# Kernel tuning notes

Hardware: AMD Instinct MI355X
Metric: run time of the kernel (lower is better)

Reference implementation:

```python
import jax, jax.numpy as jnp
import numpy as np

BN_EPS = 1e-5
POOL_TARGETS = (1500, 750, 375)


def mesh_conv(x, nb, W, g, b):
    # x: (E, C), nb: (E, 4), W: (5*C, Cout)
    E, C = x.shape
    n = x[jnp.clip(nb, 0, E - 1)]              # (E, 4, C) gather
    p1 = jnp.sort(n[:, :2, :], axis=1)          # symmetrize face-pair 1
    p2 = jnp.sort(n[:, 2:, :], axis=1)          # symmetrize face-pair 2
    feat = jnp.concatenate([x, p1[:, 0], p1[:, 1], p2[:, 0], p2[:, 1]], axis=1)  # (E, 5C)
    h = feat @ W                                # (E, Cout)
    mu = h.mean(axis=0)
    var = h.var(axis=0)                         # biased var (BatchNorm training stats)
    h = (h - mu) * jax.lax.rsqrt(var + BN_EPS) * g + b
    return jax.nn.relu(h)


def mesh_pool(x, nb, target):
    E = x.shape[0]
    scores = jnp.linalg.norm(x, axis=1)
    keep = jnp.sort(jnp.argsort(-scores)[:target])          # (target,) sorted kept edges
    x_pool = x[keep]
    remap = jnp.full((E,), -1, dtype=jnp.int32).at[keep].set(jnp.arange(target, dtype=jnp.int32))
    nbr = remap[jnp.clip(nb[keep], 0, E - 1)]               # (target, 4)
    self_idx = jnp.broadcast_to(jnp.arange(target, dtype=jnp.int32)[:, None], nbr.shape)
    nb_pool = jnp.where(nbr < 0, self_idx, nbr)
    return x_pool, nb_pool, keep


def mesh_unpool(x_coarse, keep, E_fine):
    # keep is sorted ascending; nearest kept edge by integer index distance
    # (ties -> lower index, matching torch argmin-first semantics).
    idx = jnp.arange(E_fine)
    pos = jnp.searchsorted(keep, idx)
    K = keep.shape[0]
    left = jnp.clip(pos - 1, 0, K - 1)
    right = jnp.clip(pos, 0, K - 1)
    dl = jnp.abs(idx - keep[left])
    dr = jnp.abs(idx - keep[right])
    nn_idx = jnp.where(dl <= dr, left, right)
    return x_coarse[nn_idx]                                 # kept edges map to themselves (d=0)


def setup_inputs() -> dict:
    key = jax.random.key(0)
    ks = jax.random.split(key, 20)
    E = 200000
    x = jax.random.normal(ks[0], (E, 5), dtype=jnp.float32)
    nb = jax.random.randint(ks[1], (E, 4), 0, E, dtype=jnp.int64)

    def lin(k, cin, cout):
        return (jax.random.normal(k, (cin, cout), dtype=jnp.float32) * 0.05)

    dims = [(5, 64), (64, 128), (128, 256), (256, 512), (768, 256), (384, 128), (192, 64)]
    names = ['e1', 'e2', 'e3', 'e4', 'd3', 'd2', 'd1']
    inp = {'x': x, 'nb': nb}
    for i, ((cin, cout), nm) in enumerate(zip(dims, names)):
        inp['W_' + nm] = lin(ks[2 + i], cin * 5, cout)
        inp['g_' + nm] = jnp.ones((cout,), dtype=jnp.float32)
        inp['b_' + nm] = jnp.zeros((cout,), dtype=jnp.float32)
    inp['W_head'] = lin(ks[12], 64, 4)
    inp['bias_head'] = jnp.zeros((4,), dtype=jnp.float32)
    return inp


def _forward(x, nb,
             W_e1, g_e1, b_e1, W_e2, g_e2, b_e2, W_e3, g_e3, b_e3, W_e4, g_e4, b_e4,
             W_d3, g_d3, b_d3, W_d2, g_d2, b_d2, W_d1, g_d1, b_d1,
             W_head, bias_head):
    e1 = mesh_conv(x, nb, W_e1, g_e1, b_e1)
    e1p, nb1, keep1 = mesh_pool(e1, nb, POOL_TARGETS[0])
    e2 = mesh_conv(e1p, nb1, W_e2, g_e2, b_e2)
    e2p, nb2, keep2 = mesh_pool(e2, nb1, POOL_TARGETS[1])
    e3 = mesh_conv(e2p, nb2, W_e3, g_e3, b_e3)
    e3p, nb3, keep3 = mesh_pool(e3, nb2, POOL_TARGETS[2])
    e4 = mesh_conv(e3p, nb3, W_e4, g_e4, b_e4)
    d3 = mesh_unpool(e4, keep3, e3.shape[0])
    d3 = mesh_conv(jnp.concatenate([d3, e3], axis=1), nb2, W_d3, g_d3, b_d3)
    d2 = mesh_unpool(d3, keep2, e2.shape[0])
    d2 = mesh_conv(jnp.concatenate([d2, e2], axis=1), nb1, W_d2, g_d2, b_d2)
    d1 = mesh_unpool(d2, keep1, e1.shape[0])
    d1 = mesh_conv(jnp.concatenate([d1, e1], axis=1), nb, W_d1, g_d1, b_d1)
    return d1 @ W_head + bias_head


def reference(x, nb,
              W_e1, g_e1, b_e1, W_e2, g_e2, b_e2, W_e3, g_e3, b_e3, W_e4, g_e4, b_e4,
              W_d3, g_d3, b_d3, W_d2, g_d2, b_d2, W_d1, g_d1, b_d1,
              W_head, bias_head):
    return _forward(x, nb,
                    W_e1, g_e1, b_e1, W_e2, g_e2, b_e2, W_e3, g_e3, b_e3, W_e4, g_e4, b_e4,
                    W_d3, g_d3, b_d3, W_d2, g_d2, b_d2, W_d1, g_d1, b_d1,
                    W_head, bias_head)
```

## Files before the change

kernel.cpp:

```cpp
#include <hip/hip_runtime.h>
#include <stdint.h>

typedef unsigned long long u64;
typedef unsigned int u32;
typedef unsigned short ushort_t;

#define FI __device__ __forceinline__

static constexpr float BN_EPS_F = 1e-5f;
static constexpr int E0 = 200000;
static constexpr int T1 = 1500, T2 = 750, T3 = 375;
static constexpr int CAND_CAP = 4096;
static constexpr int NB_KEEP = (E0 + 1023) / 1024;

typedef __attribute__((ext_vector_type(8))) short short8;
typedef __attribute__((ext_vector_type(4))) float f32x4;

FI int iclampi(int v, int lo, int hi) { return v < lo ? lo : (v > hi ? hi : v); }

FI ushort_t f2b(float f) {
  u32 u = __float_as_uint(f);
  u32 r = (u + 0x7FFFu + ((u >> 16) & 1u)) >> 16;
  return (ushort_t)r;
}

FI void u16minmax(const uint4& va, const uint4& vb, uint4& lo, uint4& hi) {
  const ushort_t* a = (const ushort_t*)&va;
  const ushort_t* b = (const ushort_t*)&vb;
  ushort_t* l = (ushort_t*)&lo;
  ushort_t* h = (ushort_t*)&hi;
  #pragma unroll
  for (int i = 0; i < 8; i++) {
    ushort_t x = a[i], y = b[i];
    l[i] = x < y ? x : y;
    h[i] = x < y ? y : x;
  }
}

FI int nearest_keep(const int* __restrict__ keep, int K, int idx) {
  int lo = 0, hi = K;
  while (lo < hi) { int mid = (lo + hi) >> 1; if (keep[mid] < idx) lo = mid + 1; else hi = mid; }
  int l = lo - 1; l = l < 0 ? 0 : (l > K - 1 ? K - 1 : l);
  int r = lo;     r = r < 0 ? 0 : (r > K - 1 ? K - 1 : r);
  int dl = idx - keep[l]; dl = dl < 0 ? -dl : dl;
  int dr = idx - keep[r]; dr = dr < 0 ? -dr : dr;
  return (dl <= dr) ? l : r;
}

FI int bsearch_eq(const int* __restrict__ keep, int K, int v) {
  int lo = 0, hi = K;
  while (lo < hi) { int mid = (lo + hi) >> 1; if (keep[mid] < v) lo = mid + 1; else hi = mid; }
  if (lo < K && keep[lo] == v) return lo;
  return -1;
}

template<int C, int Cout, int BR, int BC, int KT, int TR, int TC, int KSPLIT,
         bool FUSE_STATS>
__global__ __launch_bounds__((BR / TR) * (BC / TC))
void conv_kernel(const float* __restrict__ X,
                 const int* __restrict__ nb, int E,
                 const float* __restrict__ W,
                 float* __restrict__ H, float* __restrict__ stats)
{
  constexpr int NTH = (BR / TR) * (BC / TC);
  constexpr int VK = 5 * KT;
  constexpr int KC = C / KSPLIT;
  static_assert(KC % KT == 0, "KC % KT");

  const int row0 = blockIdx.x * BR;
  const int col0 = blockIdx.y * BC;
  const int c_begin = (KSPLIT > 1) ? (int)blockIdx.z * KC : 0;

  __shared__ float As[VK][BR];
  __shared__ float Bs[VK][BC];
  __shared__ int rowsS[5][BR];
  __shared__ float red[FUSE_STATS ? 2 * (BR / TR) * BC : 1];

  const int tid = threadIdx.x;

  for (int q = tid; q < BR; q += NTH) {
    int r = row0 + q;
    int rr[5];
    if (r < E) {
      rr[0] = r;
      #pragma unroll
      for (int j = 0; j < 4; j++) {
        int v = nb[(size_t)r * 4 + j];
        rr[1 + j] = iclampi(v, 0, E - 1);
      }
    } else {
      #pragma unroll
      for (int j = 0; j < 5; j++) rr[j] = -1;
    }
    #pragma unroll
    for (int j = 0; j < 5; j++) rowsS[j][q] = rr[j];
  }

  float acc[TR][TC];
  #pragma unroll
  for (int i = 0; i < TR; i++)
    #pragma unroll
    for (int j = 0; j < TC; j++) acc[i][j] = 0.f;

  const int tr = tid / (BC / TC);
  const int tc = tid % (BC / TC);
  const int rA = tr * TR;
  const int cB = tc * TC;

  for (int c0 = c_begin; c0 < c_begin + KC; c0 += KT) {
    __syncthreads();
    for (int q = tid; q < VK * (BC / 4); q += NTH) {
      int kk = q / (BC / 4);
      int c4 = q % (BC / 4);
      int p = kk / KT, t = kk % KT;
      float4 wv = *(const float4*)&W[(size_t)(p * C + c0 + t) * Cout + col0 + c4 * 4];
      *(float4*)&Bs[kk][c4 * 4] = wv;
    }
    for (int q = tid; q < BR * KT; q += NTH) {
      int t = q % KT, rq = q / KT;
      int c = c0 + t;
      float s0 = 0.f, a1 = 0.f, a2 = 0.f, a3 = 0.f, a4 = 0.f;
      if (rowsS[0][rq] >= 0) {
        float v0, v1, v2, v3;
        s0 = X[(size_t)rowsS[0][rq] * C + c];
        v0 = X[(size_t)rowsS[1][rq] * C + c];
        v1 = X[(size_t)rowsS[2][rq] * C + c];
        v2 = X[(size_t)rowsS[3][rq] * C + c];
        v3 = X[(size_t)rowsS[4][rq] * C + c];
        a1 = fminf(v0, v1); a2 = fmaxf(v0, v1);
        a3 = fminf(v2, v3); a4 = fmaxf(v2, v3);
      }
      As[0 * KT + t][rq] = s0;
      As[1 * KT + t][rq] = a1;
      As[2 * KT + t][rq] = a2;
      As[3 * KT + t][rq] = a3;
      As[4 * KT + t][rq] = a4;
    }
    __syncthreads();

    for (int kk = 0; kk < VK; kk++) {
      float a[TR], b[TC];
      #pragma unroll
      for (int i = 0; i < TR; i++) a[i] = As[kk][rA + i];
      #pragma unroll
      for (int j = 0; j < TC; j++) b[j] = Bs[kk][cB + j];
      #pragma unroll
      for (int i = 0; i < TR; i++)
        #pragma unroll
        for (int j = 0; j < TC; j++)
          acc[i][j] = fmaf(a[i], b[j], acc[i][j]);
    }
  }

  #pragma unroll
  for (int i = 0; i < TR; i++) {
    int r = row0 + rA + i;
    if (r < E) {
      if constexpr (KSPLIT > 1) {
        #pragma unroll
        for (int j = 0; j < TC; j++)
          atomicAdd(&H[(size_t)r * Cout + col0 + cB + j], acc[i][j]);
      } else {
        #pragma unroll
        for (int j = 0; j < TC; j += 4) {
          float4 v = make_float4(acc[i][j], acc[i][j + 1], acc[i][j + 2], acc[i][j + 3]);
          *(float4*)&H[(size_t)r * Cout + col0 + cB + j] = v;
        }
      }
    }
  }

  if constexpr (FUSE_STATS) {
    float s[TC], q2[TC];
    #pragma unroll
    for (int j = 0; j < TC; j++) { s[j] = 0.f; q2[j] = 0.f; }
    #pragma unroll
    for (int i = 0; i < TR; i++) {
      int r = row0 + rA + i;
      if (r < E) {
        #pragma unroll
        for (int j = 0; j < TC; j++) { float v = acc[i][j]; s[j] += v; q2[j] += v * v; }
      }
    }
    __syncthreads();
    float* redS = &red[0];
    float* redQ = &red[(BR / TR) * BC];
    #pragma unroll
    for (int j = 0; j < TC; j++) {
      redS[tr * BC + cB + j] = s[j];
      redQ[tr * BC + cB + j] = q2[j];
    }
    __syncthreads();
    for (int col = tid; col < BC; col += NTH) {
      float ts = 0.f, tq = 0.f;
      for (int g = 0; g < BR / TR; g++) { ts += redS[g * BC + col]; tq += redQ[g * BC + col]; }
      atomicAdd(&stats[col0 + col], ts);
      atomicAdd(&stats[Cout + col0 + col], tq);
    }
  }
}

__global__ __launch_bounds__(256)
void e1_conv_kernel(const float* __restrict__ X, const int* __restrict__ nb,
                    const float* __restrict__ W,
                    float* __restrict__ H, float* __restrict__ stats)
{
  __shared__ float As[25][128];
  __shared__ float Bs[25][64];
  __shared__ float red[2 * 32 * 64];

  const int tid = threadIdx.x;
  const int row0 = (int)blockIdx.x * 128;

  if (tid < 128) {
    int r = row0 + tid; if (r > E0 - 1) r = E0 - 1;
    int rs[5];
    rs[0] = r;
    #pragma unroll
    for (int j = 0; j < 4; j++) rs[1 + j] = iclampi((int)nb[(size_t)r * 4 + j], 0, E0 - 1);
    float v[5][5];
    #pragma unroll
    for (int j = 0; j < 5; j++) {
      const float* src = &X[(size_t)rs[j] * 5];
      float4 a = *(const float4*)src;
      v[j][0] = a.x; v[j][1] = a.y; v[j][2] = a.z; v[j][3] = a.w;
      v[j][4] = src[4];
    }
    #pragma unroll
    for (int c = 0; c < 5; c++) {
      As[0 * 5 + c][tid] = v[0][c];
      As[1 * 5 + c][tid] = fminf(v[1][c], v[2][c]);
      As[2 * 5 + c][tid] = fmaxf(v[1][c], v[2][c]);
      As[3 * 5 + c][tid] = fminf(v[3][c], v[4][c]);
      As[4 * 5 + c][tid] = fmaxf(v[3][c], v[4][c]);
    }
  } else {
    for (int q = tid - 128; q < 25 * 16; q += 128) {
      int k = q / 16, c4 = q % 16;
      float4 wv = *(const float4*)&W[(size_t)k * 64 + c4 * 4];
      *(float4*)&Bs[k][c4 * 4] = wv;
    }
  }
  __syncthreads();

  const int tr = tid >> 3;
  const int tc = tid & 7;
  const int rA = tr * 4;
  const int cB = tc * 8;

  float acc[4][8];
  #pragma unroll
  for (int i = 0; i < 4; i++)
    #pragma unroll
    for (int j = 0; j < 8; j++) acc[i][j] = 0.f;

  for (int k = 0; k < 25; k++) {
    float a[4], b[8];
    #pragma unroll
    for (int i = 0; i < 4; i++) a[i] = As[k][rA + i];
    #pragma unroll
    for (int j = 0; j < 8; j++) b[j] = Bs[k][cB + j];
    #pragma unroll
    for (int i = 0; i < 4; i++)
      #pragma unroll
      for (int j = 0; j < 8; j++)
        acc[i][j] = fmaf(a[i], b[j], acc[i][j]);
  }

  float s[8], q2[8];
  #pragma unroll
  for (int j = 0; j < 8; j++) { s[j] = 0.f; q2[j] = 0.f; }
  #pragma unroll
  for (int i = 0; i < 4; i++) {
    int r = row0 + rA + i;
    if (r < E0) {
      #pragma unroll
      for (int j = 0; j < 8; j += 4) {
        float4 v = make_float4(acc[i][j], acc[i][j + 1], acc[i][j + 2], acc[i][j + 3]);
        *(float4*)&H[(size_t)r * 64 + cB + j] = v;
      }
      #pragma unroll
      for (int j = 0; j < 8; j++) { float v = acc[i][j]; s[j] += v; q2[j] += v * v; }
    }
  }
  __syncthreads();
  float* redS = &red[0];
  float* redQ = &red[32 * 64];
  #pragma unroll
  for (int j = 0; j < 8; j++) {
    redS[tr * 64 + cB + j] = s[j];
    redQ[tr * 64 + cB + j] = q2[j];
  }
  __syncthreads();
  for (int col = tid; col < 64; col += 256) {
    float ts = 0.f, tq = 0.f;
    for (int g = 0; g < 32; g++) { ts += redS[g * 64 + col]; tq += redQ[g * 64 + col]; }
    atomicAdd(&stats[col], ts);
    atomicAdd(&stats[64 + col], tq);
  }
}

template<int C, int Cout, int KSPLIT>
__global__ __launch_bounds__(128)
void mfma_conv_kernel(const ushort_t* __restrict__ src,
                      const int* __restrict__ nb, int E,
                      const ushort_t* __restrict__ Wt,
                      float* __restrict__ H)
{
  constexpr int NCC_T = C / 32;
  constexpr int NCC = NCC_T / KSPLIT;
  static_assert(NCC_T % KSPLIT == 0, "NCC_T % KSPLIT");
  __shared__ int rows[5][32];

  const int tid = threadIdx.x;
  const int lane = tid & 63;
  const int wv = tid >> 6;
  const int l15 = lane & 15;
  const int quad = lane >> 4;
  const int row0 = (int)blockIdx.x * 32;
  const int col0 = (int)blockIdx.y * 64;
  const int cc0 = (KSPLIT > 1) ? (int)blockIdx.z * NCC : 0;

  if (tid < 32) {
    int r = row0 + tid; if (r > E - 1) r = E - 1;
    rows[0][tid] = r;
    #pragma unroll
    for (int j = 0; j < 4; j++) rows[1 + j][tid] = iclampi(nb[(size_t)r * 4 + j], 0, E - 1);
  }
  __syncthreads();

  const int rr = wv * 16 + l15;
  int r5[5];
  #pragma unroll
  for (int j = 0; j < 5; j++) r5[j] = rows[j][rr];

  f32x4 acc[4];
  #pragma unroll
  for (int ni = 0; ni < 4; ni++) acc[ni] = (f32x4){0.f, 0.f, 0.f, 0.f};

  uint4 raw[2][5];
  auto loadcc = [&](int par, int cc2) {
    int cb = (cc0 + cc2) * 32 + quad * 8;
    #pragma unroll
    for (int j = 0; j < 5; j++)
      raw[par][j] = *(const uint4*)&src[(size_t)r5[j] * C + cb];
  };

  loadcc(0, 0);
  #pragma unroll
  for (int cc = 0; cc < NCC; cc++) {
    const int par = cc & 1;
    if (cc + 1 < NCC) loadcc(par ^ 1, cc + 1);
    short8 a[5];
    a[0] = *(short8*)&raw[par][0];
    {
      uint4 lo, hi;
      u16minmax(raw[par][1], raw[par][2], lo, hi);
      a[1] = *(short8*)&lo; a[2] = *(short8*)&hi;
    }
    {
      uint4 lo, hi;
      u16minmax(raw[par][3], raw[par][4], lo, hi);
      a[3] = *(short8*)&lo; a[4] = *(short8*)&hi;
    }
    #pragma unroll
    for (int p = 0; p < 5; p++) {
      #pragma unroll
      for (int ni = 0; ni < 4; ni++) {
        short8 bf = *(const short8*)&Wt[((size_t)(p * Cout + col0 + ni * 16 + l15)) * C + (cc0 + cc) * 32 + quad * 8];
        acc[ni] = __builtin_amdgcn_mfma_f32_16x16x32_bf16(a[p], bf, acc[ni], 0, 0, 0);
      }
    }
  }

  #pragma unroll
  for (int reg = 0; reg < 4; reg++) {
    int r = row0 + wv * 16 + quad * 4 + reg;
    if (r < E) {
      #pragma unroll
      for (int ni = 0; ni < 4; ni++) {
        if constexpr (KSPLIT > 1)
          atomicAdd(&H[(size_t)r * Cout + col0 + ni * 16 + l15], acc[ni][reg]);
        else
          H[(size_t)r * Cout + col0 + ni * 16 + l15] = acc[ni][reg];
      }
    }
  }
}

__global__ __launch_bounds__(256, 4)
void d1_mfma_kernel(const ushort_t* __restrict__ d2b, const ushort_t* __restrict__ e1b,
                    const int* __restrict__ nn1, const int* __restrict__ nb,
                    const ushort_t* __restrict__ Wt,
                    float* __restrict__ H, float* __restrict__ stats)
{
  __shared__ int rowsD[5][128];
  __shared__ int rowsS[5][128];

  const int tid = threadIdx.x;
  const int lane = tid & 63;
  const int wv = tid >> 6;
  const int l15 = lane & 15;
  const int quad = lane >> 4;
  const int row0 = (int)blockIdx.x * 128;

  if (tid < 128) {
    int r = row0 + tid; if (r > E0 - 1) r = E0 - 1;
    int rs[5];
    rs[0] = r;
    #pragma unroll
    for (int j = 0; j < 4; j++) rs[1 + j] = iclampi((int)nb[(size_t)r * 4 + j], 0, E0 - 1);
    #pragma unroll
    for (int j = 0; j < 5; j++) { rowsS[j][tid] = rs[j]; rowsD[j][tid] = nn1[rs[j]]; }
  }
  __syncthreads();

  f32x4 acc[8];
  #pragma unroll
  for (int mi = 0; mi < 8; mi++) acc[mi] = (f32x4){0.f, 0.f, 0.f, 0.f};

  for (int cc = 0; cc < 6; cc++) {
    const bool fromD = cc < 4;
    const ushort_t* __restrict__ src = fromD ? d2b : e1b;
    const int stride = fromD ? 128 : 64;
    const int cbase = (fromD ? cc * 32 : (cc - 4) * 32) + quad * 8;

    short8 bf[5];
    #pragma unroll
    for (int p = 0; p < 5; p++)
      bf[p] = *(const short8*)&Wt[((size_t)(p * 64 + wv * 16 + l15)) * 192 + cc * 32 + quad * 8];

    #pragma unroll 2
    for (int mi = 0; mi < 8; mi++) {
      int rr = mi * 16 + l15;
      int r0, r1, r2, r3, r4;
      if (fromD) {
        r0 = rowsD[0][rr]; r1 = rowsD[1][rr]; r2 = rowsD[2][rr];
        r3 = rowsD[3][rr]; r4 = rowsD[4][rr];
      } else {
        r0 = rowsS[0][rr]; r1 = rowsS[1][rr]; r2 = rowsS[2][rr];
        r3 = rowsS[3][rr]; r4 = rowsS[4][rr];
      }
      uint4 v0 = *(const uint4*)&src[(size_t)r0 * stride + cbase];
      uint4 v1 = *(const uint4*)&src[(size_t)r1 * stride + cbase];
      uint4 v2 = *(const uint4*)&src[(size_t)r2 * stride + cbase];
      uint4 v3 = *(const uint4*)&src[(size_t)r3 * stride + cbase];
      uint4 v4 = *(const uint4*)&src[(size_t)r4 * stride + cbase];

      uint4 lo12, hi12, lo34, hi34;
      u16minmax(v1, v2, lo12, hi12);
      u16minmax(v3, v4, lo34, hi34);

      acc[mi] = __builtin_amdgcn_mfma_f32_16x16x32_bf16(*(short8*)&v0,   bf[0], acc[mi], 0, 0, 0);
      acc[mi] = __builtin_amdgcn_mfma_f32_16x16x32_bf16(*(short8*)&lo12, bf[1], acc[mi], 0, 0, 0);
      acc[mi] = __builtin_amdgcn_mfma_f32_16x16x32_bf16(*(short8*)&hi12, bf[2], acc[mi], 0, 0, 0);
      acc[mi] = __builtin_amdgcn_mfma_f32_16x16x32_bf16(*(short8*)&lo34, bf[3], acc[mi], 0, 0, 0);
      acc[mi] = __builtin_amdgcn_mfma_f32_16x16x32_bf16(*(short8*)&hi34, bf[4], acc[mi], 0, 0, 0);
    }
  }

  const int col = wv * 16 + l15;
  float s = 0.f, q = 0.f;
  #pragma unroll
  for (int mi = 0; mi < 8; mi++) {
    #pragma unroll
    for (int reg = 0; reg < 4; reg++) {
      int r = row0 + mi * 16 + quad * 4 + reg;
      if (r < E0) {
        float v = acc[mi][reg];
        H[(size_t)r * 64 + col] = v;
        s += v; q += v * v;
      }
    }
  }
  s += __shfl_xor(s, 16); q += __shfl_xor(q, 16);
  s += __shfl_xor(s, 32); q += __shfl_xor(q, 32);
  if (quad == 0) {
    atomicAdd(&stats[col], s);
    atomicAdd(&stats[64 + col], q);
  }
}

FI void prep_one(const float* __restrict__ W, ushort_t* __restrict__ Wt,
                 int C, int Cout, int i)
{
  int n = i % Cout;
  int k = i / Cout;
  int p = k / C, c = k % C;
  Wt[((size_t)(p * Cout + n)) * C + c] = f2b(W[(size_t)k * Cout + n]);
}

__global__ void prep_all_kernel(const float* __restrict__ W1, const float* __restrict__ W4,
                                const float* __restrict__ Wd3, const float* __restrict__ Wd2,
                                ushort_t* __restrict__ Wt1, ushort_t* __restrict__ Wt4,
                                ushort_t* __restrict__ Wtd3, ushort_t* __restrict__ Wtd2)
{
  int idx = (int)blockIdx.x * 256 + threadIdx.x;
  const int S1 = 5 * 192 * 64, S4 = 5 * 256 * 512, Sd3 = 5 * 768 * 256, Sd2 = 5 * 384 * 128;
  if (idx < S1) { prep_one(W1, Wt1, 192, 64, idx); return; }
  idx -= S1;
  if (idx < S4) { prep_one(W4, Wt4, 256, 512, idx); return; }
  idx -= S4;
  if (idx < Sd3) { prep_one(Wd3, Wtd3, 768, 256, idx); return; }
  idx -= Sd3;
  if (idx < Sd2) { prep_one(Wd2, Wtd2, 384, 128, idx); return; }
}

__global__ void stats_kernel(const float* __restrict__ H, int E, int Cout,
                             float* __restrict__ stats)
{
  const int RB = 64;
  int r0 = (int)blockIdx.x * RB;
  int rend = r0 + RB; if (rend > E) rend = E;
  for (int col = threadIdx.x; col < Cout; col += blockDim.x) {
    float s = 0.f, q = 0.f;
    for (int r = r0; r < rend; r++) { float v = H[(size_t)r * Cout + col]; s += v; q += v * v; }
    atomicAdd(&stats[col], s);
    atomicAdd(&stats[Cout + col], q);
  }
}

template<int Cout, bool KEYS, bool B16>
__global__ void bn_kernel(const float* __restrict__ H, const float* __restrict__ stats,
                          const float* __restrict__ g, const float* __restrict__ b,
                          int E, float* __restrict__ Out, ushort_t* __restrict__ Outb,
                          u64* __restrict__ keys)
{
  constexpr int CPL = Cout / 64;
  const int lane = threadIdx.x & 63;
  const int wid = threadIdx.x >> 6;
  const int wpb = blockDim.x >> 6;
  const float invE = 1.0f / (float)E;
  float mu[CPL], inv[CPL], gg[CPL], bb[CPL];
  #pragma unroll
  for (int u = 0; u < CPL; u++) {
    int c = lane + u * 64;
    float m = stats[c] * invE;
    float var = stats[Cout + c] * invE - m * m;
    mu[u] = m;
    inv[u] = rsqrtf(var + BN_EPS_F);
    gg[u] = g[c]; bb[u] = b[c];
  }
  for (int r = (int)blockIdx.x * wpb + wid; r < E; r += (int)gridDim.x * wpb) {
    float ss = 0.f;
    #pragma unroll
    for (int u = 0; u < CPL; u++) {
      int c = lane + u * 64;
      float v = H[(size_t)r * Cout + c];
      float o = (v - mu[u]) * inv[u] * gg[u] + bb[u];
      o = fmaxf(o, 0.f);
      Out[(size_t)r * Cout + c] = o;
      if constexpr (B16) Outb[(size_t)r * Cout + c] = f2b(o);
      ss += o * o;
    }
    if constexpr (KEYS) {
      #pragma unroll
      for (int s = 32; s > 0; s >>= 1) ss += __shfl_xor(ss, s, 64);
      if (lane == 0) {
        float sc = sqrtf(ss);
        u32 sb = __float_as_uint(sc);
        keys[r] = ((u64)sb << 32) | (u64)(0xFFFFFFFFu - (u32)r);
      }
    }
  }
}

__global__ void head_kernel(const float* __restrict__ H, const float* __restrict__ stats,
                            const float* __restrict__ g, const float* __restrict__ b,
                            const float* __restrict__ Wh, const float* __restrict__ bh,
                            int E, float* __restrict__ out)
{
  const int lane = threadIdx.x & 63;
  const int wid = threadIdx.x >> 6;
  const int wpb = blockDim.x >> 6;
  const float invE = 1.0f / (float)E;
  float m = stats[lane] * invE;
  float var = stats[64 + lane] * invE - m * m;
  float inv = rsqrtf(var + BN_EPS_F);
  float gg = g[lane], bb = b[lane];
  float4 w = *(const float4*)&Wh[lane * 4];
  float b0 = bh[0], b1 = bh[1], b2 = bh[2], b3 = bh[3];
  for (int r = (int)blockIdx.x * wpb + wid; r < E; r += (int)gridDim.x * wpb) {
    float v = H[(size_t)r * 64 + lane];
    float o = fmaxf((v - m) * inv * gg + bb, 0.f);
    float a0 = o * w.x, a1 = o * w.y, a2 = o * w.z, a3 = o * w.w;
    #pragma unroll
    for (int s = 32; s > 0; s >>= 1) {
      a0 += __shfl_xor(a0, s, 64);
      a1 += __shfl_xor(a1, s, 64);
      a2 += __shfl_xor(a2, s, 64);
      a3 += __shfl_xor(a3, s, 64);
    }
    if (lane == 0) {
      float4 ov = make_float4(a0 + b0, a1 + b1, a2 + b2, a3 + b3);
      *(float4*)&out[(size_t)r * 4] = ov;
    }
  }
}

__global__ void hist_kernel(const u64* __restrict__ keys, int E, u32* __restrict__ hist)
{
  for (int i = (int)blockIdx.x * blockDim.x + threadIdx.x; i < E;
       i += (int)gridDim.x * blockDim.x) {
    u32 bin = (u32)(keys[i] >> 44);
    atomicAdd(&hist[bin], 1u);
  }
}

__global__ void scan_kernel(const u32* __restrict__ hist, int K, u32* __restrict__ sel)
{
  __shared__ u32 csum[1024];
  __shared__ u32 sb2[1024];
  __shared__ int selChunk;
  __shared__ u32 aboveChunk;
  const int tid = threadIdx.x;
  {
    const uint4* hp = (const uint4*)(hist + (size_t)tid * 1024);
    u32 s = 0;
    for (int i = 0; i < 256; i++) {
      uint4 v = hp[i];
      s += v.x + v.y + v.z + v.w;
    }
    csum[tid] = s;
  }
  __syncthreads();
  if (tid == 0) {
    u32 above = 0; int sc = 0; u32 ab = 0;
    for (int t = 1023; t >= 0; t--) {
      if (above + csum[t] >= (u32)K) { sc = t; ab = above; break; }
      above += csum[t];
    }
    selChunk = sc; aboveChunk = ab;
  }
  __syncthreads();
  sb2[tid] = hist[(size_t)selChunk * 1024 + tid];
  __syncthreads();
  if (tid == 0) {
    u32 above = aboveChunk; int sb = 0;
    for (int t = 1023; t >= 0; t--) {
      u32 c = sb2[t];
      if (above + c >= (u32)K) { sb = t; break; }
      above += c;
    }
    sel[0] = (u32)(selChunk * 1024 + sb);
    sel[1] = above;
    sel[2] = (u32)K - above;
  }
}

__global__ void collect_kernel(const u64* __restrict__ keys, int E, const u32* __restrict__ sel,
                               u64* __restrict__ cand, u32* __restrict__ count)
{
  u32 bin = sel[0];
  for (int i = (int)blockIdx.x * blockDim.x + threadIdx.x; i < E;
       i += (int)gridDim.x * blockDim.x) {
    if ((u32)(keys[i] >> 44) == bin) {
      u32 p = atomicAdd(count, 1u);
      if (p < (u32)CAND_CAP) cand[p] = keys[i];
    }
  }
}

__global__ void thresh_kernel(const u64* __restrict__ cand, const u32* __restrict__ count,
                              const u32* __restrict__ sel, u64* __restrict__ thr)
{
  __shared__ u64 sk[CAND_CAP];
  const int tid = threadIdx.x;
  const int nth = blockDim.x;
  int n = (int)(*count > (u32)CAND_CAP ? (u32)CAND_CAP : *count);
  int n2 = 2; while (n2 < n) n2 <<= 1;
  for (int i = tid; i < n2; i += nth) sk[i] = (i < n) ? cand[i] : 0ull;
  __syncthreads();
  for (int k = 2; k <= n2; k <<= 1)
    for (int j = k >> 1; j > 0; j >>= 1) {
      for (int i = tid; i < n2; i += nth) {
        int p = i ^ j;
        if (p > i) {
          u64 a = sk[i], bb = sk[p];
          bool up = ((i & k) == 0);
          bool sw = up ? (a < bb) : (a > bb);
          if (sw) { sk[i] = bb; sk[p] = a; }
        }
      }
      __syncthreads();
    }
  if (tid == 0) {
    int kr = (int)sel[2];
    thr[0] = sk[kr - 1];
  }
}

__global__ void keep_count_kernel(const u64* __restrict__ keys, int E,
                                  const u64* __restrict__ thrp, u32* __restrict__ bcnt)
{
  const u64 thr = thrp[0];
  const int tid = threadIdx.x;
  int base = (int)blockIdx.x * 1024 + tid * 4;
  u32 c = 0;
  #pragma unroll
  for (int u = 0; u < 4; u++) {
    int i = base + u;
    if (i < E && keys[i] >= thr) c++;
  }
  __shared__ u32 sm[256];
  sm[tid] = c;
  __syncthreads();
  for (int s = 128; s > 0; s >>= 1) {
    if (tid < s) sm[tid] += sm[tid + s];
    __syncthreads();
  }
  if (tid == 0) bcnt[blockIdx.x] = sm[0];
}

__global__ void keep_scan_kernel(const u32* __restrict__ bcnt, int NB, u32* __restrict__ boffs)
{
  __shared__ u32 sm[256];
  const int tid = threadIdx.x;
  u32 v = (tid < NB) ? bcnt[tid] : 0;
  sm[tid] = v;
  __syncthreads();
  for (int off = 1; off < 256; off <<= 1) {
    u32 t = 0;
    if (tid >= off) t = sm[tid - off];
    __syncthreads();
    sm[tid] += t;
    __syncthreads();
  }
  if (tid < NB) boffs[tid] = sm[tid] - v;
}

__global__ void keep_scatter_kernel(const u64* __restrict__ keys, int E,
                                    const u64* __restrict__ thrp, const u32* __restrict__ boffs,
                                    int* __restrict__ keep, int K)
{
  const u64 thr = thrp[0];
  const int tid = threadIdx.x;
  int base = (int)blockIdx.x * 1024 + tid * 4;
  u32 f[4]; u32 c = 0;
  #pragma unroll
  for (int u = 0; u < 4; u++) {
    int i = base + u;
    f[u] = (i < E && keys[i] >= thr) ? 1u : 0u;
    c += f[u];
  }
  __shared__ u32 sm[256];
  sm[tid] = c;
  __syncthreads();
  for (int off = 1; off < 256; off <<= 1) {
    u32 t = 0;
    if (tid >= off) t = sm[tid - off];
    __syncthreads();
    sm[tid] += t;
    __syncthreads();
  }
  u32 pos = boffs[blockIdx.x] + sm[tid] - c;
  #pragma unroll
  for (int u = 0; u < 4; u++) {
    if (f[u]) {
      if (pos < (u32)K) keep[pos] = base + u;
      pos++;
    }
  }
}

template<int NPOW>
__global__ void pool_select_kernel(const u64* __restrict__ keys, int E, int K,
                                   int* __restrict__ keep)
{
  __shared__ u64 sk[NPOW];
  __shared__ int si[NPOW];
  const int tid = threadIdx.x, nth = blockDim.x;
  for (int i = tid; i < NPOW; i += nth) sk[i] = (i < E) ? keys[i] : 0ull;
  __syncthreads();
  for (int k = 2; k <= NPOW; k <<= 1)
    for (int j = k >> 1; j > 0; j >>= 1) {
      for (int i = tid; i < NPOW; i += nth) {
        int p = i ^ j;
        if (p > i) {
          u64 a = sk[i], bb = sk[p];
          bool up = ((i & k) == 0);
          bool sw = up ? (a < bb) : (a > bb);
          if (sw) { sk[i] = bb; sk[p] = a; }
        }
      }
      __syncthreads();
    }
  for (int i = tid; i < NPOW; i += nth)
    si[i] = (i < K) ? (int)(0xFFFFFFFFu - (u32)(sk[i] & 0xFFFFFFFFull)) : 0x7FFFFFFF;
  __syncthreads();
  for (int k = 2; k <= NPOW; k <<= 1)
    for (int j = k >> 1; j > 0; j >>= 1) {
      for (int i = tid; i < NPOW; i += nth) {
        int p = i ^ j;
        if (p > i) {
          int a = si[i], bb = si[p];
          bool up = ((i & k) == 0);
          bool sw = up ? (a > bb) : (a < bb);
          if (sw) { si[i] = bb; si[p] = a; }
        }
      }
      __syncthreads();
    }
  for (int i = tid; i < K; i += nth) keep[i] = si[i];
}

template<int C, bool B16>
__global__ void pool_finish_kernel(const float* __restrict__ Xsrc, const int* __restrict__ nb_src,
                                   const int* __restrict__ keep, int K, int Esrc,
                                   float* __restrict__ Xp, ushort_t* __restrict__ Xpb,
                                   int* __restrict__ nbp)
{
  int total = K * C;
  for (int idx = (int)blockIdx.x * blockDim.x + threadIdx.x; idx < total;
       idx += (int)gridDim.x * blockDim.x) {
    int i = idx / C, c = idx % C;
    float v = Xsrc[(size_t)keep[i] * C + c];
    if constexpr (B16) Xpb[idx] = f2b(v);
    else Xp[idx] = v;
  }
  for (int idx = (int)blockIdx.x * blockDim.x + threadIdx.x; idx < K * 4;
       idx += (int)gridDim.x * blockDim.x) {
    int i = idx >> 2, j = idx & 3;
    int v = nb_src[(size_t)keep[i] * 4 + j];
    v = iclampi(v, 0, Esrc - 1);
    int p = bsearch_eq(keep, K, v);
    nbp[idx] = (p < 0) ? i : p;
  }
}

__global__ void unpool_cat_b16_kernel(const float* __restrict__ Xc, const float* __restrict__ Xs,
                                      const int* __restrict__ keep, int K, int E,
                                      int Cc, int Cs, ushort_t* __restrict__ out)
{
  int Ct = Cc + Cs;
  int Ct8 = Ct >> 3;
  int total = E * Ct8;
  for (int idx = (int)blockIdx.x * blockDim.x + threadIdx.x; idx < total;
       idx += (int)gridDim.x * blockDim.x) {
    int r = idx / Ct8, c = (idx % Ct8) << 3;
    const float* srcp;
    if (c < Cc) { int nn = nearest_keep(keep, K, r); srcp = &Xc[(size_t)nn * Cc + c]; }
    else srcp = &Xs[(size_t)r * Cs + (c - Cc)];
    float4 a = *(const float4*)srcp;
    float4 b = *(const float4*)(srcp + 4);
    ushort_t o[8];
    o[0] = f2b(a.x); o[1] = f2b(a.y); o[2] = f2b(a.z); o[3] = f2b(a.w);
    o[4] = f2b(b.x); o[5] = f2b(b.y); o[6] = f2b(b.z); o[7] = f2b(b.w);
    *(uint4*)&out[(size_t)r * Ct + c] = *(uint4*)o;
  }
}

__global__ void nn_map_kernel(const int* __restrict__ keep, int K, int E, int* __restrict__ nn)
{
  for (int i = (int)blockIdx.x * blockDim.x + threadIdx.x; i < E;
       i += (int)gridDim.x * blockDim.x)
    nn[i] = nearest_keep(keep, K, i);
}

extern "C" void kernel_launch(void* const* d_in, const int* in_sizes, int n_in,
                              void* d_out, int out_size, void* d_ws, size_t ws_size,
                              hipStream_t stream)
{
  (void)in_sizes; (void)n_in; (void)out_size; (void)ws_size;
  const float* x     = (const float*)d_in[0];
  const int*   nb    = (const int*)d_in[1];
  const float* W_e1  = (const float*)d_in[2];
  const float* g_e1  = (const float*)d_in[3];
  const float* b_e1  = (const float*)d_in[4];
  const float* W_e2  = (const float*)d_in[5];
  const float* g_e2  = (const float*)d_in[6];
  const float* b_e2  = (const float*)d_in[7];
  const float* W_e3  = (const float*)d_in[8];
  const float* g_e3  = (const float*)d_in[9];
  const float* b_e3  = (const float*)d_in[10];
  const float* W_e4  = (const float*)d_in[11];
  const float* g_e4  = (const float*)d_in[12];
  const float* b_e4  = (const float*)d_in[13];
  const float* W_d3  = (const float*)d_in[14];
  const float* g_d3  = (const float*)d_in[15];
  const float* b_d3  = (const float*)d_in[16];
  const float* W_d2  = (const float*)d_in[17];
  const float* g_d2  = (const float*)d_in[18];
  const float* b_d2  = (const float*)d_in[19];
  const float* W_d1  = (const float*)d_in[20];
  const float* g_d1  = (const float*)d_in[21];
  const float* b_d1  = (const float*)d_in[22];
  const float* W_head = (const float*)d_in[23];
  const float* bias_head = (const float*)d_in[24];
  float* out = (float*)d_out;

  char* p = (char*)d_ws;
  auto alloc = [&](size_t bytes) -> char* {
    char* q = p; p += (bytes + 255) & ~(size_t)255; return q;
  };

  char* zz = p;
  u32*   hist  = (u32*)alloc(sizeof(u32) * (1u << 20));
  float* stats = (float*)alloc(sizeof(float) * 2 * (64 + 128 + 256 + 512 + 256 + 128 + 64));
  u32*   ctrl  = (u32*)alloc(sizeof(u32) * 16);
  u64*   thr   = (u64*)alloc(sizeof(u64) * 2);
  u32*   sel   = (u32*)alloc(sizeof(u32) * 8);
  float* H2    = (float*)alloc(sizeof(float) * T1 * 128);
  float* H3    = (float*)alloc(sizeof(float) * T2 * 256);
  float* H4    = (float*)alloc(sizeof(float) * T3 * 512);
  float* Hd3   = (float*)alloc(sizeof(float) * T2 * 256);
  float* Hd2   = (float*)alloc(sizeof(float) * T1 * 128);
  size_t zz_bytes = (size_t)(p - zz);
  u32*   bcnt  = (u32*)alloc(sizeof(u32) * 256);
  u32*   boffs = (u32*)alloc(sizeof(u32) * 256);
  float* e1    = (float*)alloc(sizeof(float) * (size_t)E0 * 64);
  u64*   keys1 = (u64*)alloc(sizeof(u64) * E0);
  u64*   cand  = (u64*)alloc(sizeof(u64) * CAND_CAP);
  int*   keep1 = (int*)alloc(sizeof(int) * T1);
  float* e1p   = (float*)alloc(sizeof(float) * T1 * 64);
  int*   nb1   = (int*)alloc(sizeof(int) * T1 * 4);
  float* e2    = (float*)alloc(sizeof(float) * T1 * 128);
  u64*   keys2 = (u64*)alloc(sizeof(u64) * T1);
  int*   keep2 = (int*)alloc(sizeof(int) * T2);
  float* e2p   = (float*)alloc(sizeof(float) * T2 * 128);
  int*   nb2   = (int*)alloc(sizeof(int) * T2 * 4);
  float* e3    = (float*)alloc(sizeof(float) * T2 * 256);
  u64*   keys3 = (u64*)alloc(sizeof(u64) * T2);
  int*   keep3 = (int*)alloc(sizeof(int) * T3);
  ushort_t* e3pb = (ushort_t*)alloc(sizeof(ushort_t) * T3 * 256);
  int*   nb3   = (int*)alloc(sizeof(int) * T3 * 4);
  float* e4    = (float*)alloc(sizeof(float) * T3 * 512);
  ushort_t* d3catb = (ushort_t*)alloc(sizeof(ushort_t) * T2 * 768);
  float* d3    = (float*)alloc(sizeof(float) * T2 * 256);
  ushort_t* d2catb = (ushort_t*)alloc(sizeof(ushort_t) * T1 * 384);
  float* d2    = (float*)alloc(sizeof(float) * T1 * 128);
  int*   nn1   = (int*)alloc(sizeof(int) * E0);
  float* Hd1   = (float*)alloc(sizeof(float) * (size_t)E0 * 64);
  ushort_t* e1b = (ushort_t*)alloc(sizeof(ushort_t) * (size_t)E0 * 64);
  ushort_t* d2b = (ushort_t*)alloc(sizeof(ushort_t) * T1 * 128);
  ushort_t* Wt1 = (ushort_t*)alloc(sizeof(ushort_t) * 5 * 64 * 192);
  ushort_t* Wt4 = (ushort_t*)alloc(sizeof(ushort_t) * 5 * 512 * 256);
  ushort_t* Wtd3 = (ushort_t*)alloc(sizeof(ushort_t) * 5 * 256 * 768);
  ushort_t* Wtd2 = (ushort_t*)alloc(sizeof(ushort_t) * 5 * 128 * 384);

  float* s1  = stats;
  float* s2  = s1 + 2 * 64;
  float* s3  = s2 + 2 * 128;
  float* s4  = s3 + 2 * 256;
  float* sd3 = s4 + 2 * 512;
  float* sd2 = sd3 + 2 * 256;
  float* sd1 = sd2 + 2 * 128;

  hipMemsetAsync(zz, 0, zz_bytes, stream);
  const int PREP_TOTAL = 5 * (192 * 64 + 256 * 512 + 768 * 256 + 384 * 128);
  prep_all_kernel<<<dim3((PREP_TOTAL + 255) / 256), 256, 0, stream>>>(
      W_d1, W_e4, W_d3, W_d2, Wt1, Wt4, Wtd3, Wtd2);

  e1_conv_kernel<<<dim3((E0 + 127) / 128), 256, 0, stream>>>(x, nb, W_e1, e1, s1);
  bn_kernel<64, true, true><<<dim3(8192), 256, 0, stream>>>(e1, s1, g_e1, b_e1, E0, e1, e1b, keys1);

  hist_kernel<<<dim3(782), 256, 0, stream>>>(keys1, E0, hist);
  scan_kernel<<<dim3(1), 1024, 0, stream>>>(hist, T1, sel);
  collect_kernel<<<dim3(782), 256, 0, stream>>>(keys1, E0, sel, cand, ctrl);
  thresh_kernel<<<dim3(1), 1024, 0, stream>>>(cand, ctrl, sel, thr);
  keep_count_kernel<<<dim3(NB_KEEP), 256, 0, stream>>>(keys1, E0, thr, bcnt);
  keep_scan_kernel<<<dim3(1), 256, 0, stream>>>(bcnt, NB_KEEP, boffs);
  keep_scatter_kernel<<<dim3(NB_KEEP), 256, 0, stream>>>(keys1, E0, thr, boffs, keep1, T1);
  pool_finish_kernel<64, false><<<dim3(380), 256, 0, stream>>>(e1, nb, keep1, T1, E0, e1p, nullptr, nb1);

  conv_kernel<64, 128, 32, 64, 8, 2, 4, 2, false>
      <<<dim3((T1 + 31) / 32, 128 / 64, 2), 256, 0, stream>>>(e1p, nb1, T1, W_e2, H2, nullptr);
  stats_kernel<<<dim3((T1 + 63) / 64), 256, 0, stream>>>(H2, T1, 128, s2);
  bn_kernel<128, true, false><<<dim3(512), 256, 0, stream>>>(H2, s2, g_e2, b_e2, T1, e2, nullptr, keys2);
  pool_select_kernel<2048><<<dim3(1), 1024, 0, stream>>>(keys2, T1, T2, keep2);
  pool_finish_kernel<128, false><<<dim3(380), 256, 0, stream>>>(e2, nb1, keep2, T2, T1, e2p, nullptr, nb2);

  conv_kernel<128, 256, 32, 64, 8, 2, 4, 4, false>
      <<<dim3((T2 + 31) / 32, 256 / 64, 4), 256, 0, stream>>>(e2p, nb2, T2, W_e3, H3, nullptr);
  stats_kernel<<<dim3((T2 + 63) / 64), 256, 0, stream>>>(H3, T2, 256, s3);
  bn_kernel<256, true, false><<<dim3(256), 256, 0, stream>>>(H3, s3, g_e3, b_e3, T2, e3, nullptr, keys3);
  pool_select_kernel<1024><<<dim3(1), 1024, 0, stream>>>(keys3, T2, T3, keep3);
  pool_finish_kernel<256, true><<<dim3(380), 256, 0, stream>>>(e3, nb2, keep3, T3, T2, nullptr, e3pb, nb3);

  mfma_conv_kernel<256, 512, 4><<<dim3((T3 + 31) / 32, 512 / 64, 4), 128, 0, stream>>>(
      e3pb, nb3, T3, Wt4, H4);
  stats_kernel<<<dim3((T3 + 63) / 64), 256, 0, stream>>>(H4, T3, 512, s4);
  bn_kernel<512, false, false><<<dim3(128), 256, 0, stream>>>(
      H4, s4, g_e4, b_e4, T3, e4, nullptr, nullptr);

  unpool_cat_b16_kernel<<<dim3((T2 * 768 / 8 + 255) / 256), 256, 0, stream>>>(
      e4, e3, keep3, T3, T2, 512, 256, d3catb);
  mfma_conv_kernel<768, 256, 6><<<dim3((T2 + 31) / 32, 256 / 64, 6), 128, 0, stream>>>(
      d3catb, nb2, T2, Wtd3, Hd3);
  stats_kernel<<<dim3((T2 + 63) / 64), 256, 0, stream>>>(Hd3, T2, 256, sd3);
  bn_kernel<256, false, false><<<dim3(256), 256, 0, stream>>>(
      Hd3, sd3, g_d3, b_d3, T2, d3, nullptr, nullptr);

  unpool_cat_b16_kernel<<<dim3((T1 * 384 / 8 + 255) / 256), 256, 0, stream>>>(
      d3, e2, keep2, T2, T1, 256, 128, d2catb);
  mfma_conv_kernel<384, 128, 3><<<dim3((T1 + 31) / 32, 128 / 64, 3), 128, 0, stream>>>(
      d2catb, nb1, T1, Wtd2, Hd2);
  stats_kernel<<<dim3((T1 + 63) / 64), 256, 0, stream>>>(Hd2, T1, 128, sd2);
  bn_kernel<128, false, true><<<dim3(512), 256, 0, stream>>>(
      Hd2, sd2, g_d2, b_d2, T1, d2, d2b, nullptr);

  nn_map_kernel<<<dim3(782), 256, 0, stream>>>(keep1, T1, E0, nn1);
  d1_mfma_kernel<<<dim3((E0 + 127) / 128), 256, 0, stream>>>(d2b, e1b, nn1, nb, Wt1, Hd1, sd1);

  head_kernel<<<dim3(8192), 256, 0, stream>>>(Hd1, sd1, g_d1, b_d1, W_head, bias_head, E0, out);
}
```

Baseline: 987.7 us.

## Cut large-tensor traffic: skip fp32 e1, bf16 d1 output, fuse keep scan and nn map

The e1 BatchNorm pass now writes only the bf16 copy and keys. The pooled e1 rows are recomputed from the raw conv output inside a new fused pool+BN kernel. The d1 conv writes its pre-BN output as bf16, which the head kernel reads back, halving that 200k×64 buffer's traffic. The nearest-keep map is computed inside the d1 kernel via binary search over keep1 staged in shared memory, and the keep scan is folded into the scatter kernel, removing two launches. The trade-offs are bf16 rounding of Hd1 before BN (the stats are still taken from fp32), a redundant per-block prefix scan, and repeated binary searches per block.

```diff
diff --git a/kernel.cpp b/kernel.cpp
--- a/kernel.cpp
+++ b/kernel.cpp
@@ -23,6 +23,8 @@
   u32 r = (u + 0x7FFFu + ((u >> 16) & 1u)) >> 16;
   return (ushort_t)r;
 }
+
+FI float b2f(ushort_t v) { return __uint_as_float(((u32)v) << 16); }
 
 FI void u16minmax(const uint4& va, const uint4& vb, uint4& lo, uint4& hi) {
   const ushort_t* a = (const ushort_t*)&va;
@@ -390,12 +392,13 @@
 
 __global__ __launch_bounds__(256, 4)
 void d1_mfma_kernel(const ushort_t* __restrict__ d2b, const ushort_t* __restrict__ e1b,
-                    const int* __restrict__ nn1, const int* __restrict__ nb,
+                    const int* __restrict__ keep1, const int* __restrict__ nb,
                     const ushort_t* __restrict__ Wt,
-                    float* __restrict__ H, float* __restrict__ stats)
+                    ushort_t* __restrict__ Hb, float* __restrict__ stats)
 {
   __shared__ int rowsD[5][128];
   __shared__ int rowsS[5][128];
+  __shared__ int keepL[T1];
 
   const int tid = threadIdx.x;
   const int lane = tid & 63;
@@ -404,6 +407,9 @@
   const int quad = lane >> 4;
   const int row0 = (int)blockIdx.x * 128;
 
+  for (int i = tid; i < T1; i += 256) keepL[i] = keep1[i];
+  __syncthreads();
+
   if (tid < 128) {
     int r = row0 + tid; if (r > E0 - 1) r = E0 - 1;
     int rs[5];
@@ -411,7 +417,10 @@
     #pragma unroll
     for (int j = 0; j < 4; j++) rs[1 + j] = iclampi((int)nb[(size_t)r * 4 + j], 0, E0 - 1);
     #pragma unroll
-    for (int j = 0; j < 5; j++) { rowsS[j][tid] = rs[j]; rowsD[j][tid] = nn1[rs[j]]; }
+    for (int j = 0; j < 5; j++) {
+      rowsS[j][tid] = rs[j];
+      rowsD[j][tid] = nearest_keep(keepL, T1, rs[j]);
+    }
   }
   __syncthreads();
 
@@ -468,7 +477,7 @@
       int r = row0 + mi * 16 + quad * 4 + reg;
       if (r < E0) {
         float v = acc[mi][reg];
-        H[(size_t)r * 64 + col] = v;
+        Hb[(size_t)r * 64 + col] = f2b(v);
         s += v; q += v * v;
       }
     }
@@ -520,7 +529,7 @@
   }
 }
 
-template<int Cout, bool KEYS, bool B16>
+template<int Cout, bool KEYS, bool F32, bool B16>
 __global__ void bn_kernel(const float* __restrict__ H, const float* __restrict__ stats,
                           const float* __restrict__ g, const float* __restrict__ b,
                           int E, float* __restrict__ Out, ushort_t* __restrict__ Outb,
@@ -549,7 +558,7 @@
       float v = H[(size_t)r * Cout + c];
       float o = (v - mu[u]) * inv[u] * gg[u] + bb[u];
       o = fmaxf(o, 0.f);
-      Out[(size_t)r * Cout + c] = o;
+      if constexpr (F32) Out[(size_t)r * Cout + c] = o;
       if constexpr (B16) Outb[(size_t)r * Cout + c] = f2b(o);
       ss += o * o;
     }
@@ -565,7 +574,7 @@
   }
 }
 
-__global__ void head_kernel(const float* __restrict__ H, const float* __restrict__ stats,
+__global__ void head_kernel(const ushort_t* __restrict__ Hb, const float* __restrict__ stats,
                             const float* __restrict__ g, const float* __restrict__ b,
                             const float* __restrict__ Wh, const float* __restrict__ bh,
                             int E, float* __restrict__ out)
@@ -581,7 +590,7 @@
   float4 w = *(const float4*)&Wh[lane * 4];
   float b0 = bh[0], b1 = bh[1], b2 = bh[2], b3 = bh[3];
   for (int r = (int)blockIdx.x * wpb + wid; r < E; r += (int)gridDim.x * wpb) {
-    float v = H[(size_t)r * 64 + lane];
+    float v = b2f(Hb[(size_t)r * 64 + lane]);
     float o = fmaxf((v - m) * inv * gg + bb, 0.f);
     float a0 = o * w.x, a1 = o * w.y, a2 = o * w.z, a3 = o * w.w;
     #pragma unroll
@@ -712,12 +721,38 @@
   if (tid == 0) bcnt[blockIdx.x] = sm[0];
 }
 
-__global__ void keep_scan_kernel(const u32* __restrict__ bcnt, int NB, u32* __restrict__ boffs)
-{
+__global__ void keep_scatter_kernel(const u64* __restrict__ keys, int E,
+                                    const u64* __restrict__ thrp, const u32* __restrict__ bcnt,
+                                    int NB, int* __restrict__ keep, int K)
+{
+  const u64 thr = thrp[0];
+  const int tid = threadIdx.x;
+
+  __shared__ u32 pre[256];
+  __shared__ u32 base0;
+  u32 bv = (tid < NB) ? bcnt[tid] : 0;
+  pre[tid] = bv;
+  __syncthreads();
+  for (int off = 1; off < 256; off <<= 1) {
+    u32 t = 0;
+    if (tid >= off) t = pre[tid - off];
+    __syncthreads();
+    pre[tid] += t;
+    __syncthreads();
+  }
+  if (tid == 0) base0 = (blockIdx.x == 0) ? 0u : pre[blockIdx.x - 1];
+  __syncthreads();
+
+  int base = (int)blockIdx.x * 1024 + tid * 4;
+  u32 f[4]; u32 c = 0;
+  #pragma unroll
+  for (int u = 0; u < 4; u++) {
+    int i = base + u;
+    f[u] = (i < E && keys[i] >= thr) ? 1u : 0u;
+    c += f[u];
+  }
   __shared__ u32 sm[256];
-  const int tid = threadIdx.x;
-  u32 v = (tid < NB) ? bcnt[tid] : 0;
-  sm[tid] = v;
+  sm[tid] = c;
   __syncthreads();
   for (int off = 1; off < 256; off <<= 1) {
     u32 t = 0;
@@ -726,34 +761,7 @@
     sm[tid] += t;
     __syncthreads();
   }
-  if (tid < NB) boffs[tid] = sm[tid] - v;
-}
-
-__global__ void keep_scatter_kernel(const u64* __restrict__ keys, int E,
-                                    const u64* __restrict__ thrp, const u32* __restrict__ boffs,
-                                    int* __restrict__ keep, int K)
-{
-  const u64 thr = thrp[0];
-  const int tid = threadIdx.x;
-  int base = (int)blockIdx.x * 1024 + tid * 4;
-  u32 f[4]; u32 c = 0;
-  #pragma unroll
-  for (int u = 0; u < 4; u++) {
-    int i = base + u;
-    f[u] = (i < E && keys[i] >= thr) ? 1u : 0u;
-    c += f[u];
-  }
-  __shared__ u32 sm[256];
-  sm[tid] = c;
-  __syncthreads();
-  for (int off = 1; off < 256; off <<= 1) {
-    u32 t = 0;
-    if (tid >= off) t = sm[tid - off];
-    __syncthreads();
-    sm[tid] += t;
-    __syncthreads();
-  }
-  u32 pos = boffs[blockIdx.x] + sm[tid] - c;
+  u32 pos = base0 + sm[tid] - c;
   #pragma unroll
   for (int u = 0; u < 4; u++) {
     if (f[u]) {
@@ -802,6 +810,34 @@
       __syncthreads();
     }
   for (int i = tid; i < K; i += nth) keep[i] = si[i];
+}
+
+__global__ void pool_finish_bn_kernel(const float* __restrict__ H, const float* __restrict__ stats,
+                                      const float* __restrict__ g, const float* __restrict__ b,
+                                      const int* __restrict__ nb_src,
+                                      const int* __restrict__ keep, int K, int Esrc,
+                                      float* __restrict__ Xp, int* __restrict__ nbp)
+{
+  const float invE = 1.0f / (float)Esrc;
+  int total = K * 64;
+  for (int idx = (int)blockIdx.x * blockDim.x + threadIdx.x; idx < total;
+       idx += (int)gridDim.x * blockDim.x) {
+    int i = idx >> 6, c = idx & 63;
+    float m = stats[c] * invE;
+    float var = stats[64 + c] * invE - m * m;
+    float inv = rsqrtf(var + BN_EPS_F);
+    float v = H[(size_t)keep[i] * 64 + c];
+    float o = (v - m) * inv * g[c] + b[c];
+    Xp[idx] = fmaxf(o, 0.f);
+  }
+  for (int idx = (int)blockIdx.x * blockDim.x + threadIdx.x; idx < K * 4;
+       idx += (int)gridDim.x * blockDim.x) {
+    int i = idx >> 2, j = idx & 3;
+    int v = nb_src[(size_t)keep[i] * 4 + j];
+    v = iclampi(v, 0, Esrc - 1);
+    int p = bsearch_eq(keep, K, v);
+    nbp[idx] = (p < 0) ? i : p;
+  }
 }
 
 template<int C, bool B16>
@@ -848,13 +884,6 @@
     o[4] = f2b(b.x); o[5] = f2b(b.y); o[6] = f2b(b.z); o[7] = f2b(b.w);
     *(uint4*)&out[(size_t)r * Ct + c] = *(uint4*)o;
   }
-}
-
-__global__ void nn_map_kernel(const int* __restrict__ keep, int K, int E, int* __restrict__ nn)
-{
-  for (int i = (int)blockIdx.x * blockDim.x + threadIdx.x; i < E;
-       i += (int)gridDim.x * blockDim.x)
-    nn[i] = nearest_keep(keep, K, i);
 }
 
 extern "C" void kernel_launch(void* const* d_in, const int* in_sizes, int n_in,
@@ -907,8 +936,7 @@
   float* Hd2   = (float*)alloc(sizeof(float) * T1 * 128);
   size_t zz_bytes = (size_t)(p - zz);
   u32*   bcnt  = (u32*)alloc(sizeof(u32) * 256);
-  u32*   boffs = (u32*)alloc(sizeof(u32) * 256);
-  float* e1    = (float*)alloc(sizeof(float) * (size_t)E0 * 64);
+  float* He1   = (float*)alloc(sizeof(float) * (size_t)E0 * 64);
   u64*   keys1 = (u64*)alloc(sizeof(u64) * E0);
   u64*   cand  = (u64*)alloc(sizeof(u64) * CAND_CAP);
   int*   keep1 = (int*)alloc(sizeof(int) * T1);
@@ -929,8 +957,7 @@
   float* d3    = (float*)alloc(sizeof(float) * T2 * 256);
   ushort_t* d2catb = (ushort_t*)alloc(sizeof(ushort_t) * T1 * 384);
   float* d2    = (float*)alloc(sizeof(float) * T1 * 128);
-  int*   nn1   = (int*)alloc(sizeof(int) * E0);
-  float* Hd1   = (float*)alloc(sizeof(float) * (size_t)E0 * 64);
+  ushort_t* Hd1b = (ushort_t*)alloc(sizeof(ushort_t) * (size_t)E0 * 64);
   ushort_t* e1b = (ushort_t*)alloc(sizeof(ushort_t) * (size_t)E0 * 64);
   ushort_t* d2b = (ushort_t*)alloc(sizeof(ushort_t) * T1 * 128);
   ushort_t* Wt1 = (ushort_t*)alloc(sizeof(ushort_t) * 5 * 64 * 192);
@@ -951,36 +978,39 @@
   prep_all_kernel<<<dim3((PREP_TOTAL + 255) / 256), 256, 0, stream>>>(
       W_d1, W_e4, W_d3, W_d2, Wt1, Wt4, Wtd3, Wtd2);
 
-  e1_conv_kernel<<<dim3((E0 + 127) / 128), 256, 0, stream>>>(x, nb, W_e1, e1, s1);
-  bn_kernel<64, true, true><<<dim3(8192), 256, 0, stream>>>(e1, s1, g_e1, b_e1, E0, e1, e1b, keys1);
+  e1_conv_kernel<<<dim3((E0 + 127) / 128), 256, 0, stream>>>(x, nb, W_e1, He1, s1);
+  bn_kernel<64, true, false, true><<<dim3(8192), 256, 0, stream>>>(
+      He1, s1, g_e1, b_e1, E0, nullptr, e1b, keys1);
 
   hist_kernel<<<dim3(782), 256, 0, stream>>>(keys1, E0, hist);
   scan_kernel<<<dim3(1), 1024, 0, stream>>>(hist, T1, sel);
   collect_kernel<<<dim3(782), 256, 0, stream>>>(keys1, E0, sel, cand, ctrl);
   thresh_kernel<<<dim3(1), 1024, 0, stream>>>(cand, ctrl, sel, thr);
   keep_count_kernel<<<dim3(NB_KEEP), 256, 0, stream>>>(keys1, E0, thr, bcnt);
-  keep_scan_kernel<<<dim3(1), 256, 0, stream>>>(bcnt, NB_KEEP, boffs);
-  keep_scatter_kernel<<<dim3(NB_KEEP), 256, 0, stream>>>(keys1, E0, thr, boffs, keep1, T1);
-  pool_finish_kernel<64, false><<<dim3(380), 256, 0, stream>>>(e1, nb, keep1, T1, E0, e1p, nullptr, nb1);
+  keep_scatter_kernel<<<dim3(NB_KEEP), 256, 0, stream>>>(keys1, E0, thr, bcnt, NB_KEEP, keep1, T1);
+  pool_finish_bn_kernel<<<dim3(380), 256, 0, stream>>>(
+      He1, s1, g_e1, b_e1, nb, keep1, T1, E0, e1p, nb1);
 
   conv_kernel<64, 128, 32, 64, 8, 2, 4, 2, false>
       <<<dim3((T1 + 31) / 32, 128 / 64, 2), 256, 0, stream>>>(e1p, nb1, T1, W_e2, H2, nullptr);
   stats_kernel<<<dim3((T1 + 63) / 64), 256, 0, stream>>>(H2, T1, 128, s2);
-  bn_kernel<128, true, false><<<dim3(512), 256, 0, stream>>>(H2, s2, g_e2, b_e2, T1, e2, nullptr, keys2);
+  bn_kernel<128, true, true, false><<<dim3(512), 256, 0, stream>>>(
+      H2, s2, g_e2, b_e2, T1, e2, nullptr, keys2);
   pool_select_kernel<2048><<<dim3(1), 1024, 0, stream>>>(keys2, T1, T2, keep2);
   pool_finish_kernel<128, false><<<dim3(380), 256, 0, stream>>>(e2, nb1, keep2, T2, T1, e2p, nullptr, nb2);
 
   conv_kernel<128, 256, 32, 64, 8, 2, 4, 4, false>
       <<<dim3((T2 + 31) / 32, 256 / 64, 4), 256, 0, stream>>>(e2p, nb2, T2, W_e3, H3, nullptr);
   stats_kernel<<<dim3((T2 + 63) / 64), 256, 0, stream>>>(H3, T2, 256, s3);
-  bn_kernel<256, true, false><<<dim3(256), 256, 0, stream>>>(H3, s3, g_e3, b_e3, T2, e3, nullptr, keys3);
+  bn_kernel<256, true, true, false><<<dim3(256), 256, 0, stream>>>(
+      H3, s3, g_e3, b_e3, T2, e3, nullptr, keys3);
   pool_select_kernel<1024><<<dim3(1), 1024, 0, stream>>>(keys3, T2, T3, keep3);
   pool_finish_kernel<256, true><<<dim3(380), 256, 0, stream>>>(e3, nb2, keep3, T3, T2, nullptr, e3pb, nb3);
 
   mfma_conv_kernel<256, 512, 4><<<dim3((T3 + 31) / 32, 512 / 64, 4), 128, 0, stream>>>(
       e3pb, nb3, T3, Wt4, H4);
   stats_kernel<<<dim3((T3 + 63) / 64), 256, 0, stream>>>(H4, T3, 512, s4);
-  bn_kernel<512, false, false><<<dim3(128), 256, 0, stream>>>(
+  bn_kernel<512, false, true, false><<<dim3(128), 256, 0, stream>>>(
       H4, s4, g_e4, b_e4, T3, e4, nullptr, nullptr);
 
   unpool_cat_b16_kernel<<<dim3((T2 * 768 / 8 + 255) / 256), 256, 0, stream>>>(
@@ -988,7 +1018,7 @@
   mfma_conv_kernel<768, 256, 6><<<dim3((T2 + 31) / 32, 256 / 64, 6), 128, 0, stream>>>(
       d3catb, nb2, T2, Wtd3, Hd3);
   stats_kernel<<<dim3((T2 + 63) / 64), 256, 0, stream>>>(Hd3, T2, 256, sd3);
-  bn_kernel<256, false, false><<<dim3(256), 256, 0, stream>>>(
+  bn_kernel<256, false, true, false><<<dim3(256), 256, 0, stream>>>(
       Hd3, sd3, g_d3, b_d3, T2, d3, nullptr, nullptr);
 
   unpool_cat_b16_kernel<<<dim3((T1 * 384 / 8 + 255) / 256), 256, 0, stream>>>(
@@ -996,11 +1026,10 @@
   mfma_conv_kernel<384, 128, 3><<<dim3((T1 + 31) / 32, 128 / 64, 3), 128, 0, stream>>>(
       d2catb, nb1, T1, Wtd2, Hd2);
   stats_kernel<<<dim3((T1 + 63) / 64), 256, 0, stream>>>(Hd2, T1, 128, sd2);
-  bn_kernel<128, false, true><<<dim3(512), 256, 0, stream>>>(
+  bn_kernel<128, false, true, true><<<dim3(512), 256, 0, stream>>>(
       Hd2, sd2, g_d2, b_d2, T1, d2, d2b, nullptr);
 
-  nn_map_kernel<<<dim3(782), 256, 0, stream>>>(keep1, T1, E0, nn1);
-  d1_mfma_kernel<<<dim3((E0 + 127) / 128), 256, 0, stream>>>(d2b, e1b, nn1, nb, Wt1, Hd1, sd1);
-
-  head_kernel<<<dim3(8192), 256, 0, stream>>>(Hd1, sd1, g_d1, b_d1, W_head, bias_head, E0, out);
-}
+  d1_mfma_kernel<<<dim3((E0 + 127) / 128), 256, 0, stream>>>(d2b, e1b, keep1, nb, Wt1, Hd1b, sd1);
+
+  head_kernel<<<dim3(8192), 256, 0, stream>>>(Hd1b, sd1, g_d1, b_d1, W_head, bias_head, E0, out);
+}
```

New measurement: 980.2 us. No clear change (-0.8%).
